# Kernel optimization log

Measured on AMD Instinct MI355X. Metric: run time of the kernel, lower is better.

## Reference

```python
import math
import jax, jax.numpy as jnp
import numpy as np

B = 64
INPUT_SIZE = 10080
PATCH = 18
S = INPUT_SIZE // PATCH  # 560 patches
E = 96                    # embed_dim
H = 12                    # num_heads
D = 96                    # head_dim == embed_dim (PAT quirk)
F = 256                   # ff_dim
L = 2                     # num_layers
EPS = 1e-5


def _sinusoidal_pe(seq_len, embed_dim):
    pos = jnp.arange(seq_len, dtype=jnp.float32)[:, None]
    div = jnp.exp(jnp.arange(0, embed_dim, 2, dtype=jnp.float32) * (-math.log(10000.0) / embed_dim))
    pe = jnp.zeros((seq_len, embed_dim), dtype=jnp.float32)
    pe = pe.at[:, 0::2].set(jnp.sin(pos * div))
    pe = pe.at[:, 1::2].set(jnp.cos(pos * div))
    return pe


def _layernorm(x, g, b):
    mu = jnp.mean(x, axis=-1, keepdims=True)
    var = jnp.var(x, axis=-1, keepdims=True)
    return (x - mu) * jax.lax.rsqrt(var + EPS) * g + b


def setup_inputs() -> dict:
    key = jax.random.key(0)
    ks = jax.random.split(key, 12)
    sd = 0.02
    inp = {
        "x": jax.random.normal(ks[0], (B, INPUT_SIZE), dtype=jnp.float32),
        "patch_W": jax.random.normal(ks[1], (PATCH, E), dtype=jnp.float32) * sd,
        "patch_b": jnp.zeros((E,), jnp.float32),
        "Wq": jax.random.normal(ks[2], (L, H, E, D), dtype=jnp.float32) * sd,
        "bq": jnp.zeros((L, H, D), jnp.float32),
        "Wk": jax.random.normal(ks[3], (L, H, E, D), dtype=jnp.float32) * sd,
        "bk": jnp.zeros((L, H, D), jnp.float32),
        "Wv": jax.random.normal(ks[4], (L, H, E, D), dtype=jnp.float32) * sd,
        "bv": jnp.zeros((L, H, D), jnp.float32),
        "Wo": jax.random.normal(ks[5], (L, H * D, E), dtype=jnp.float32) * sd,
        "bo": jnp.zeros((L, E), jnp.float32),
        "ff1_W": jax.random.normal(ks[6], (L, E, F), dtype=jnp.float32) * sd,
        "ff1_b": jnp.zeros((L, F), jnp.float32),
        "ff2_W": jax.random.normal(ks[7], (L, F, E), dtype=jnp.float32) * sd,
        "ff2_b": jnp.zeros((L, E), jnp.float32),
        "n1_g": jnp.ones((L, E), jnp.float32),
        "n1_b": jnp.zeros((L, E), jnp.float32),
        "n2_g": jnp.ones((L, E), jnp.float32),
        "n2_b": jnp.zeros((L, E), jnp.float32),
    }
    return inp


def reference(x, patch_W, patch_b, Wq, bq, Wk, bk, Wv, bv, Wo, bo,
              ff1_W, ff1_b, ff2_W, ff2_b, n1_g, n1_b, n2_g, n2_b):
    scale = 1.0 / math.sqrt(D)
    # patch embedding: [B, S, PATCH] -> [B, S, E]
    h = x.reshape(B, S, PATCH) @ patch_W + patch_b
    h = h + _sinusoidal_pe(S, E)[None]
    for l in range(L):
        # all heads at once (original loops over heads; same math)
        q = jnp.einsum('bse,hed->bhsd', h, Wq[l]) + bq[l][None, :, None, :]
        k = jnp.einsum('bse,hed->bhsd', h, Wk[l]) + bk[l][None, :, None, :]
        v = jnp.einsum('bse,hed->bhsd', h, Wv[l]) + bv[l][None, :, None, :]
        scores = jnp.einsum('bhsd,bhtd->bhst', q, k) * scale
        attn = jax.nn.softmax(scores, axis=-1)
        heads = jnp.einsum('bhst,bhtd->bhsd', attn, v)
        concat = heads.transpose(0, 2, 1, 3).reshape(B, S, H * D)
        attn_out = concat @ Wo[l] + bo[l]
        h = _layernorm(h + attn_out, n1_g[l], n1_b[l])
        ff = jax.nn.relu(h @ ff1_W[l] + ff1_b[l]) @ ff2_W[l] + ff2_b[l]
        h = _layernorm(h + ff, n2_g[l], n2_b[l])
    return h
```

## Files before the change

kernel.cpp:

```cpp
#include <hip/hip_runtime.h>
#include <hip/hip_bf16.h>
#include <math.h>

#define BATCH 64
#define CHUNK 32
#define INPUT_SIZE 10080
#define PATCH 18
#define SEQ 560
#define EMB 96
#define NHEAD 12
#define HDIM 96
#define FFDIM 256
#define NLAYER 2
#define TOK (BATCH * SEQ)
#define EPSV 1e-5f
#define SCALE 0.10206207261596577f

typedef __attribute__((ext_vector_type(8))) short bf16x8;
typedef __attribute__((ext_vector_type(4))) short bf16x4;
typedef __attribute__((ext_vector_type(4))) float f32x4;

static __device__ __forceinline__ short f2bf(float x) {
  union { __hip_bfloat16 b; short s; } u;
  u.b = __float2bfloat16(x);
  return u.s;
}

__global__ __launch_bounds__(256) void allprep_kernel(
    const float* __restrict__ Wq, const float* __restrict__ Wk,
    const float* __restrict__ Wv, const float* __restrict__ Wo,
    const float* __restrict__ ff1_W, const float* __restrict__ ff2_W,
    __hip_bfloat16* __restrict__ wqT, __hip_bfloat16* __restrict__ wkvT,
    __hip_bfloat16* __restrict__ woT, __hip_bfloat16* __restrict__ ff1WT,
    __hip_bfloat16* __restrict__ ff2WT) {
  int bx = blockIdx.x;
  if (bx < 72) {
    int hh = bx % NHEAD, mat = (bx / NHEAD) % 3, l = bx / 36;
    const float* src = (mat == 0 ? Wq : (mat == 1 ? Wk : Wv)) +
                       ((size_t)l * NHEAD + hh) * EMB * HDIM;
    __shared__ float t[HDIM * 97];
    for (int i = threadIdx.x; i < EMB * HDIM; i += 256) {
      int e = i / HDIM, d = i % HDIM;
      t[d * 97 + e] = src[i];
    }
    __syncthreads();
    __hip_bfloat16* dst;
    if (mat == 0)
      dst = wqT + ((size_t)l * NHEAD + hh) * HDIM * EMB;
    else
      dst = wkvT + ((size_t)l * 2 * NHEAD * HDIM + (mat - 1) * NHEAD * HDIM +
                    hh * HDIM) * EMB;
    for (int j = threadIdx.x; j < HDIM * EMB; j += 256) {
      int d = j / EMB, e = j % EMB;
      dst[j] = __float2bfloat16(t[d * 97 + e]);
    }
  } else if (bx < 74) {
    int l = bx - 72;
    const float* src = Wo + (size_t)l * NHEAD * HDIM * EMB;
    __hip_bfloat16* dst = woT + (size_t)l * EMB * NHEAD * HDIM;
    for (int i = threadIdx.x; i < EMB * NHEAD * HDIM; i += 256) {
      int e = i / (NHEAD * HDIM), j = i % (NHEAD * HDIM);
      dst[i] = __float2bfloat16(src[(size_t)j * EMB + e]);
    }
  } else {
    int idx = bx - 74;
    int mat = idx % 2, l = idx / 2;
    if (mat == 0) {
      const float* src = ff1_W + (size_t)l * EMB * FFDIM;
      __hip_bfloat16* dst = ff1WT + (size_t)l * FFDIM * EMB;
      for (int i = threadIdx.x; i < FFDIM * EMB; i += 256) {
        int f = i / EMB, e = i % EMB;
        dst[i] = __float2bfloat16(src[(size_t)e * FFDIM + f]);
      }
    } else {
      const float* src = ff2_W + (size_t)l * FFDIM * EMB;
      __hip_bfloat16* dst = ff2WT + (size_t)l * EMB * FFDIM;
      for (int i = threadIdx.x; i < EMB * FFDIM; i += 256) {
        int e = i / FFDIM, f = i % FFDIM;
        dst[i] = __float2bfloat16(src[(size_t)f * EMB + e]);
      }
    }
  }
}

__global__ void patch_pe_kernel(const float* __restrict__ x,
                                const float* __restrict__ W,
                                const float* __restrict__ bias,
                                float* __restrict__ h,
                                __hip_bfloat16* __restrict__ hbf) {
  int gid = blockIdx.x * blockDim.x + threadIdx.x;
  if (gid >= TOK * EMB) return;
  int tok = gid / EMB;
  int e = gid % EMB;
  int b = tok / SEQ;
  int s = tok % SEQ;
  const float* xp = x + b * INPUT_SIZE + s * PATCH;
  float acc = bias[e];
#pragma unroll
  for (int p = 0; p < PATCH; p++) acc += xp[p] * W[p * EMB + e];
  int i = e >> 1;
  float freq = __expf(-(float)(2 * i) * (9.210340371976184f / 96.0f));
  float ang = (float)s * freq;
  acc += (e & 1) ? cosf(ang) : sinf(ang);
  h[gid] = acc;
  hbf[gid] = __float2bfloat16(acc);
}

__global__ __launch_bounds__(256) void kv_mfma_kernel(
    const __hip_bfloat16* __restrict__ hbf,
    const __hip_bfloat16* __restrict__ wkvT, const float* __restrict__ bk,
    const float* __restrict__ bv, __hip_bfloat16* __restrict__ kbuf,
    __hip_bfloat16* __restrict__ vbufT, int b0) {
  const int wave = threadIdx.x >> 6;
  const int lane = threadIdx.x & 63;
  const int tq = lane & 15;
  const int quad = lane >> 4;
  const int m0 = blockIdx.x * 64 + wave * 16;
  const int n0 = blockIdx.y * 64;

  __shared__ short tile[4][16][68];

  const short* ap =
      (const short*)hbf + ((size_t)b0 * SEQ + m0 + tq) * EMB + quad * 8;
  bf16x8 a0 = *(const bf16x8*)(ap);
  bf16x8 a1 = *(const bf16x8*)(ap + 32);
  bf16x8 a2 = *(const bf16x8*)(ap + 64);

  f32x4 acc[4];
  const f32x4 zero4 = {0.f, 0.f, 0.f, 0.f};
#pragma unroll
  for (int nt = 0; nt < 4; nt++) acc[nt] = zero4;
#pragma unroll
  for (int nt = 0; nt < 4; nt++) {
    const short* bp =
        (const short*)wkvT + (size_t)(n0 + nt * 16 + tq) * EMB + quad * 8;
    bf16x8 b0f = *(const bf16x8*)(bp);
    bf16x8 b1f = *(const bf16x8*)(bp + 32);
    bf16x8 b2f = *(const bf16x8*)(bp + 64);
    acc[nt] = __builtin_amdgcn_mfma_f32_16x16x32_bf16(a0, b0f, acc[nt], 0, 0, 0);
    acc[nt] = __builtin_amdgcn_mfma_f32_16x16x32_bf16(a1, b1f, acc[nt], 0, 0, 0);
    acc[nt] = __builtin_amdgcn_mfma_f32_16x16x32_bf16(a2, b2f, acc[nt], 0, 0, 0);
  }

  const int tl0 = m0 + quad * 4;
  const int blb = tl0 / SEQ;
  const int ss0 = tl0 - blb * SEQ;

  if (n0 < NHEAD * HDIM) {
#pragma unroll
    for (int nt = 0; nt < 4; nt++) {
      int n = n0 + nt * 16 + tq;
      float bias = bk[n];
#pragma unroll
      for (int j = 0; j < 4; j++)
        tile[wave][quad * 4 + j][nt * 16 + tq] = f2bf(acc[nt][j] + bias);
    }
#pragma unroll
    for (int it = 0; it < 2; it++) {
      int idx = it * 64 + lane;
      int row = idx >> 3;
      int seg = idx & 7;
      int tl = m0 + row;
      int bb = tl / SEQ;
      int ss = tl - bb * SEQ;
      int r0s = n0 + seg * 8;
      int hh2 = r0s / HDIM;
      int d0 = r0s - hh2 * HDIM;
      bf16x8 v = *(const bf16x8*)&tile[wave][row][seg * 8];
      *(bf16x8*)((short*)kbuf +
                 ((size_t)(bb * NHEAD + hh2) * SEQ + ss) * HDIM + d0) = v;
    }
  } else {
#pragma unroll
    for (int nt = 0; nt < 4; nt++) {
      int n = n0 + nt * 16 + tq;
      int r = n - NHEAD * HDIM;
      int hh2 = r / HDIM;
      int d = r - hh2 * HDIM;
      float bias = bv[r];
      bf16x4 pack;
#pragma unroll
      for (int j = 0; j < 4; j++) pack[j] = f2bf(acc[nt][j] + bias);
      *(bf16x4*)((short*)vbufT +
                 ((size_t)(blb * NHEAD + hh2) * HDIM + d) * SEQ + ss0) = pack;
    }
  }
}

#define PSTRIDE 584
#define KSTR 104
__global__ __launch_bounds__(256, 2) void attn_mfma_kernel(
    const __hip_bfloat16* __restrict__ hbf,
    const __hip_bfloat16* __restrict__ wqT, const float* __restrict__ bq,
    const __hip_bfloat16* __restrict__ kbuf,
    const __hip_bfloat16* __restrict__ vbufT,
    __hip_bfloat16* __restrict__ heads, int b0) {
  const int flat = blockIdx.x;
  const int xcd = flat & 7;
  const int slot = flat >> 3;
  const int g = (slot / 9) * 8 + xcd;
  const int qt = slot % 9;
  const int hh = g % NHEAD;
  const int bl = g / NHEAD;
  const int wave = threadIdx.x >> 6;
  const int lane = threadIdx.x & 63;
  const int tq = lane & 15;
  const int quad = lane >> 4;

  __shared__ __align__(16) short sbuf[4 * 16 * PSTRIDE];
  short* pw = sbuf + wave * 16 * PSTRIDE;

  const size_t bh = (size_t)(bl * NHEAD + hh);
  const short* kb = (const short*)kbuf + bh * SEQ * HDIM;
  const short* vb = (const short*)vbufT + bh * HDIM * SEQ;

  const int q0 = qt * 64 + wave * 16;
  int qrow = q0 + tq;
  if (qrow > SEQ - 1) qrow = SEQ - 1;
  const short* hp =
      (const short*)hbf + ((size_t)(b0 + bl) * SEQ + qrow) * EMB + quad * 8;
  bf16x8 ha0 = *(const bf16x8*)(hp);
  bf16x8 ha1 = *(const bf16x8*)(hp + 32);
  bf16x8 ha2 = *(const bf16x8*)(hp + 64);
  const f32x4 zero4 = {0.f, 0.f, 0.f, 0.f};
  f32x4 qacc[6];
#pragma unroll
  for (int dt = 0; dt < 6; dt++) qacc[dt] = zero4;
#pragma unroll
  for (int dt = 0; dt < 6; dt++) {
    const short* wp = (const short*)wqT +
                      ((size_t)hh * HDIM + dt * 16 + tq) * EMB + quad * 8;
    bf16x8 w0 = *(const bf16x8*)(wp);
    bf16x8 w1 = *(const bf16x8*)(wp + 32);
    bf16x8 w2 = *(const bf16x8*)(wp + 64);
    qacc[dt] = __builtin_amdgcn_mfma_f32_16x16x32_bf16(ha0, w0, qacc[dt], 0, 0, 0);
    qacc[dt] = __builtin_amdgcn_mfma_f32_16x16x32_bf16(ha1, w1, qacc[dt], 0, 0, 0);
    qacc[dt] = __builtin_amdgcn_mfma_f32_16x16x32_bf16(ha2, w2, qacc[dt], 0, 0, 0);
  }
#pragma unroll
  for (int dt = 0; dt < 6; dt++) {
    int d = dt * 16 + tq;
    float bias = bq[hh * HDIM + d];
#pragma unroll
    for (int r = 0; r < 4; r++)
      pw[(quad * 4 + r) * PSTRIDE + d] = f2bf((qacc[dt][r] + bias) * SCALE);
  }
  bf16x8 aq0 = *(const bf16x8*)&pw[tq * PSTRIDE + quad * 8];
  bf16x8 aq1 = *(const bf16x8*)&pw[tq * PSTRIDE + quad * 8 + 32];
  bf16x8 aq2 = *(const bf16x8*)&pw[tq * PSTRIDE + quad * 8 + 64];
  __syncthreads();

  f32x4 acc[35];
#pragma unroll
  for (int tt = 0; tt < 35; tt++) acc[tt] = zero4;

  for (int i = threadIdx.x; i < 288 * 12; i += 256) {
    int row = i / 12, gg = i - row * 12;
    *(bf16x8*)&sbuf[row * KSTR + gg * 8] =
        *(const bf16x8*)(kb + (size_t)row * HDIM + gg * 8);
  }
  __syncthreads();
#pragma unroll
  for (int tt = 0; tt < 18; tt++) {
    const short* kp = &sbuf[(tt * 16 + tq) * KSTR + quad * 8];
    bf16x8 kb0 = *(const bf16x8*)(kp);
    bf16x8 kb1 = *(const bf16x8*)(kp + 32);
    bf16x8 kb2 = *(const bf16x8*)(kp + 64);
    acc[tt] = __builtin_amdgcn_mfma_f32_16x16x32_bf16(aq0, kb0, acc[tt], 0, 0, 0);
    acc[tt] = __builtin_amdgcn_mfma_f32_16x16x32_bf16(aq1, kb1, acc[tt], 0, 0, 0);
    acc[tt] = __builtin_amdgcn_mfma_f32_16x16x32_bf16(aq2, kb2, acc[tt], 0, 0, 0);
  }
  __syncthreads();

  for (int i = threadIdx.x; i < 272 * 12; i += 256) {
    int row = i / 12, gg = i - row * 12;
    *(bf16x8*)&sbuf[row * KSTR + gg * 8] =
        *(const bf16x8*)(kb + (size_t)(288 + row) * HDIM + gg * 8);
  }
  __syncthreads();
#pragma unroll
  for (int tt = 18; tt < 35; tt++) {
    const short* kp = &sbuf[(tt * 16 + tq - 288) * KSTR + quad * 8];
    bf16x8 kb0 = *(const bf16x8*)(kp);
    bf16x8 kb1 = *(const bf16x8*)(kp + 32);
    bf16x8 kb2 = *(const bf16x8*)(kp + 64);
    acc[tt] = __builtin_amdgcn_mfma_f32_16x16x32_bf16(aq0, kb0, acc[tt], 0, 0, 0);
    acc[tt] = __builtin_amdgcn_mfma_f32_16x16x32_bf16(aq1, kb1, acc[tt], 0, 0, 0);
    acc[tt] = __builtin_amdgcn_mfma_f32_16x16x32_bf16(aq2, kb2, acc[tt], 0, 0, 0);
  }

  float m0 = -1e30f, m1 = -1e30f, m2 = -1e30f, m3 = -1e30f;
#pragma unroll
  for (int tt = 0; tt < 35; tt++) {
    m0 = fmaxf(m0, acc[tt][0]);
    m1 = fmaxf(m1, acc[tt][1]);
    m2 = fmaxf(m2, acc[tt][2]);
    m3 = fmaxf(m3, acc[tt][3]);
  }
#pragma unroll
  for (int mask = 1; mask < 16; mask <<= 1) {
    m0 = fmaxf(m0, __shfl_xor(m0, mask, 64));
    m1 = fmaxf(m1, __shfl_xor(m1, mask, 64));
    m2 = fmaxf(m2, __shfl_xor(m2, mask, 64));
    m3 = fmaxf(m3, __shfl_xor(m3, mask, 64));
  }
  float l0 = 0.f, l1 = 0.f, l2 = 0.f, l3 = 0.f;
#pragma unroll
  for (int tt = 0; tt < 35; tt++) {
    float p0 = __expf(acc[tt][0] - m0); acc[tt][0] = p0; l0 += p0;
    float p1 = __expf(acc[tt][1] - m1); acc[tt][1] = p1; l1 += p1;
    float p2 = __expf(acc[tt][2] - m2); acc[tt][2] = p2; l2 += p2;
    float p3 = __expf(acc[tt][3] - m3); acc[tt][3] = p3; l3 += p3;
  }
#pragma unroll
  for (int mask = 1; mask < 16; mask <<= 1) {
    l0 += __shfl_xor(l0, mask, 64);
    l1 += __shfl_xor(l1, mask, 64);
    l2 += __shfl_xor(l2, mask, 64);
    l3 += __shfl_xor(l3, mask, 64);
  }
  __syncthreads();

  for (int i = lane; i < 256; i += 64)
    pw[(i >> 4) * PSTRIDE + 560 + (i & 15)] = 0;
#pragma unroll
  for (int tt = 0; tt < 35; tt++) {
    int col = tt * 16 + tq;
    pw[(quad * 4 + 0) * PSTRIDE + col] = f2bf(acc[tt][0]);
    pw[(quad * 4 + 1) * PSTRIDE + col] = f2bf(acc[tt][1]);
    pw[(quad * 4 + 2) * PSTRIDE + col] = f2bf(acc[tt][2]);
    pw[(quad * 4 + 3) * PSTRIDE + col] = f2bf(acc[tt][3]);
  }

  f32x4 oacc[6];
#pragma unroll
  for (int dt = 0; dt < 6; dt++) oacc[dt] = zero4;
#pragma unroll
  for (int kt = 0; kt < 18; kt++) {
    bf16x8 pa = *(const bf16x8*)&pw[tq * PSTRIDE + kt * 32 + quad * 8];
#pragma unroll
    for (int dt = 0; dt < 6; dt++) {
      const short* vp = vb + (size_t)(dt * 16 + tq) * SEQ + kt * 32 + quad * 8;
      bf16x8 vf = *(const bf16x8*)vp;
      oacc[dt] = __builtin_amdgcn_mfma_f32_16x16x32_bf16(pa, vf, oacc[dt], 0, 0, 0);
    }
  }

  float r0 = 1.f / l0, r1 = 1.f / l1, r2 = 1.f / l2, r3 = 1.f / l3;
  int qg = q0 + quad * 4;
  __hip_bfloat16* hpout =
      heads + ((size_t)(b0 + bl) * SEQ) * (NHEAD * HDIM) + (size_t)hh * HDIM;
#pragma unroll
  for (int dt = 0; dt < 6; dt++) {
    int d = dt * 16 + tq;
    if (qg + 0 < SEQ) hpout[(size_t)(qg + 0) * (NHEAD * HDIM) + d] = __float2bfloat16(oacc[dt][0] * r0);
    if (qg + 1 < SEQ) hpout[(size_t)(qg + 1) * (NHEAD * HDIM) + d] = __float2bfloat16(oacc[dt][1] * r1);
    if (qg + 2 < SEQ) hpout[(size_t)(qg + 2) * (NHEAD * HDIM) + d] = __float2bfloat16(oacc[dt][2] * r2);
    if (qg + 3 < SEQ) hpout[(size_t)(qg + 3) * (NHEAD * HDIM) + d] = __float2bfloat16(oacc[dt][3] * r3);
  }
}

__global__ __launch_bounds__(256) void wo_ln_mfma_kernel(
    const __hip_bfloat16* __restrict__ heads,
    const __hip_bfloat16* __restrict__ woT, const float* __restrict__ bo,
    const float* __restrict__ gamma, const float* __restrict__ beta,
    const float* __restrict__ hres, float* __restrict__ hA,
    __hip_bfloat16* __restrict__ hbf) {
  const int wave = threadIdx.x >> 6;
  const int lane = threadIdx.x & 63;
  const int tq = lane & 15;
  const int quad = lane >> 4;
  const int m0 = blockIdx.x * 64 + wave * 16;

  const short* ap = (const short*)heads + (size_t)(m0 + tq) * (NHEAD * HDIM);
  const short* bp = (const short*)woT;

  f32x4 acc[6];
  const f32x4 zero4 = {0.f, 0.f, 0.f, 0.f};
#pragma unroll
  for (int dt = 0; dt < 6; dt++) acc[dt] = zero4;

  for (int kt = 0; kt < 36; kt++) {
    bf16x8 af = *(const bf16x8*)(ap + kt * 32 + quad * 8);
#pragma unroll
    for (int dt = 0; dt < 6; dt++) {
      bf16x8 bfr = *(const bf16x8*)(bp + (size_t)(dt * 16 + tq) * (NHEAD * HDIM) +
                                    kt * 32 + quad * 8);
      acc[dt] = __builtin_amdgcn_mfma_f32_16x16x32_bf16(af, bfr, acc[dt], 0, 0, 0);
    }
  }

  const int tok0 = m0 + quad * 4;
  float s1[4] = {0.f, 0.f, 0.f, 0.f};
  float s2[4] = {0.f, 0.f, 0.f, 0.f};
#pragma unroll
  for (int dt = 0; dt < 6; dt++) {
    int n = dt * 16 + tq;
    float bias = bo[n];
#pragma unroll
    for (int r = 0; r < 4; r++) {
      float val = acc[dt][r] + bias + hres[(size_t)(tok0 + r) * EMB + n];
      acc[dt][r] = val;
      s1[r] += val;
      s2[r] += val * val;
    }
  }
#pragma unroll
  for (int mask = 1; mask < 16; mask <<= 1) {
#pragma unroll
    for (int r = 0; r < 4; r++) {
      s1[r] += __shfl_xor(s1[r], mask, 64);
      s2[r] += __shfl_xor(s2[r], mask, 64);
    }
  }
  float mean[4], rstd[4];
#pragma unroll
  for (int r = 0; r < 4; r++) {
    mean[r] = s1[r] * (1.0f / EMB);
    float var = s2[r] * (1.0f / EMB) - mean[r] * mean[r];
    rstd[r] = rsqrtf(var + EPSV);
  }
#pragma unroll
  for (int dt = 0; dt < 6; dt++) {
    int n = dt * 16 + tq;
    float g = gamma[n], bt = beta[n];
#pragma unroll
    for (int r = 0; r < 4; r++) {
      float o = (acc[dt][r] - mean[r]) * rstd[r] * g + bt;
      hA[(size_t)(tok0 + r) * EMB + n] = o;
      hbf[(size_t)(tok0 + r) * EMB + n] = __float2bfloat16(o);
    }
  }
}

__global__ __launch_bounds__(256) void ff1_mfma_kernel(
    const __hip_bfloat16* __restrict__ hbf,
    const __hip_bfloat16* __restrict__ ff1WT, const float* __restrict__ b1,
    __hip_bfloat16* __restrict__ ffbf) {
  const int wave = threadIdx.x >> 6;
  const int lane = threadIdx.x & 63;
  const int tq = lane & 15;
  const int quad = lane >> 4;
  const int m0 = blockIdx.x * 64 + wave * 16;

  const short* ap = (const short*)hbf + (size_t)(m0 + tq) * EMB + quad * 8;
  bf16x8 a0 = *(const bf16x8*)(ap);
  bf16x8 a1 = *(const bf16x8*)(ap + 32);
  bf16x8 a2 = *(const bf16x8*)(ap + 64);

  f32x4 acc[16];
  const f32x4 zero4 = {0.f, 0.f, 0.f, 0.f};
#pragma unroll
  for (int nt = 0; nt < 16; nt++) acc[nt] = zero4;
#pragma unroll
  for (int nt = 0; nt < 16; nt++) {
    const short* bp =
        (const short*)ff1WT + (size_t)(nt * 16 + tq) * EMB + quad * 8;
    bf16x8 b0f = *(const bf16x8*)(bp);
    bf16x8 b1f = *(const bf16x8*)(bp + 32);
    bf16x8 b2f = *(const bf16x8*)(bp + 64);
    acc[nt] = __builtin_amdgcn_mfma_f32_16x16x32_bf16(a0, b0f, acc[nt], 0, 0, 0);
    acc[nt] = __builtin_amdgcn_mfma_f32_16x16x32_bf16(a1, b1f, acc[nt], 0, 0, 0);
    acc[nt] = __builtin_amdgcn_mfma_f32_16x16x32_bf16(a2, b2f, acc[nt], 0, 0, 0);
  }

  const int tok0 = m0 + quad * 4;
#pragma unroll
  for (int nt = 0; nt < 16; nt++) {
    int n = nt * 16 + tq;
    float bias = b1[n];
#pragma unroll
    for (int r = 0; r < 4; r++) {
      ffbf[(size_t)(tok0 + r) * FFDIM + n] =
          __float2bfloat16(fmaxf(acc[nt][r] + bias, 0.f));
    }
  }
}

__global__ __launch_bounds__(256) void ff2_ln_mfma_kernel(
    const __hip_bfloat16* __restrict__ ffbf,
    const __hip_bfloat16* __restrict__ ff2WT, const float* __restrict__ b2,
    const float* __restrict__ gamma, const float* __restrict__ beta,
    const float* __restrict__ hres, float* __restrict__ hout,
    __hip_bfloat16* __restrict__ hbf_out) {
  const int wave = threadIdx.x >> 6;
  const int lane = threadIdx.x & 63;
  const int tq = lane & 15;
  const int quad = lane >> 4;
  const int m0 = blockIdx.x * 64 + wave * 16;

  const short* ap = (const short*)ffbf + (size_t)(m0 + tq) * FFDIM;
  const short* bp = (const short*)ff2WT;

  f32x4 acc[6];
  const f32x4 zero4 = {0.f, 0.f, 0.f, 0.f};
#pragma unroll
  for (int dt = 0; dt < 6; dt++) acc[dt] = zero4;

#pragma unroll
  for (int kt = 0; kt < 8; kt++) {
    bf16x8 af = *(const bf16x8*)(ap + kt * 32 + quad * 8);
#pragma unroll
    for (int dt = 0; dt < 6; dt++) {
      bf16x8 bfr = *(const bf16x8*)(bp + (size_t)(dt * 16 + tq) * FFDIM +
                                    kt * 32 + quad * 8);
      acc[dt] = __builtin_amdgcn_mfma_f32_16x16x32_bf16(af, bfr, acc[dt], 0, 0, 0);
    }
  }

  const int tok0 = m0 + quad * 4;
  float s1[4] = {0.f, 0.f, 0.f, 0.f};
  float s2[4] = {0.f, 0.f, 0.f, 0.f};
#pragma unroll
  for (int dt = 0; dt < 6; dt++) {
    int n = dt * 16 + tq;
    float bias = b2[n];
#pragma unroll
    for (int r = 0; r < 4; r++) {
      float val = acc[dt][r] + bias + hres[(size_t)(tok0 + r) * EMB + n];
      acc[dt][r] = val;
      s1[r] += val;
      s2[r] += val * val;
    }
  }
#pragma unroll
  for (int mask = 1; mask < 16; mask <<= 1) {
#pragma unroll
    for (int r = 0; r < 4; r++) {
      s1[r] += __shfl_xor(s1[r], mask, 64);
      s2[r] += __shfl_xor(s2[r], mask, 64);
    }
  }
  float mean[4], rstd[4];
#pragma unroll
  for (int r = 0; r < 4; r++) {
    mean[r] = s1[r] * (1.0f / EMB);
    float var = s2[r] * (1.0f / EMB) - mean[r] * mean[r];
    rstd[r] = rsqrtf(var + EPSV);
  }
#pragma unroll
  for (int dt = 0; dt < 6; dt++) {
    int n = dt * 16 + tq;
    float g = gamma[n], bt = beta[n];
#pragma unroll
    for (int r = 0; r < 4; r++) {
      float o = (acc[dt][r] - mean[r]) * rstd[r] * g + bt;
      hout[(size_t)(tok0 + r) * EMB + n] = o;
      hbf_out[(size_t)(tok0 + r) * EMB + n] = __float2bfloat16(o);
    }
  }
}

extern "C" void kernel_launch(void* const* d_in, const int* in_sizes, int n_in,
                              void* d_out, int out_size, void* d_ws,
                              size_t ws_size, hipStream_t stream) {
  const float* x = (const float*)d_in[0];
  const float* patch_W = (const float*)d_in[1];
  const float* patch_b = (const float*)d_in[2];
  const float* Wq = (const float*)d_in[3];
  const float* bq = (const float*)d_in[4];
  const float* Wk = (const float*)d_in[5];
  const float* bk = (const float*)d_in[6];
  const float* Wv = (const float*)d_in[7];
  const float* bv = (const float*)d_in[8];
  const float* Wo = (const float*)d_in[9];
  const float* bo = (const float*)d_in[10];
  const float* ff1_W = (const float*)d_in[11];
  const float* ff1_b = (const float*)d_in[12];
  const float* ff2_W = (const float*)d_in[13];
  const float* ff2_b = (const float*)d_in[14];
  const float* n1_g = (const float*)d_in[15];
  const float* n1_b = (const float*)d_in[16];
  const float* n2_g = (const float*)d_in[17];
  const float* n2_b = (const float*)d_in[18];

  const size_t h_bytes = (size_t)TOK * EMB * sizeof(float);
  const size_t hbf_bytes = (size_t)TOK * EMB * 2;
  const size_t kv_bytes = (size_t)CHUNK * NHEAD * SEQ * HDIM * 2;
  const size_t heads_bytes = (size_t)TOK * NHEAD * HDIM * 2;
  const size_t wqT_bytes = (size_t)NLAYER * NHEAD * HDIM * EMB * 2;
  const size_t wkvT_bytes = 2 * wqT_bytes;
  const size_t woT_bytes = (size_t)NLAYER * EMB * NHEAD * HDIM * 2;
  const size_t ffw_bytes = (size_t)NLAYER * FFDIM * EMB * 2;
  char* ws = (char*)d_ws;
  size_t off = 0;
  float* h = (float*)(ws + off); off += h_bytes;
  float* hA = (float*)(ws + off); off += h_bytes;
  __hip_bfloat16* hbf = (__hip_bfloat16*)(ws + off); off += hbf_bytes;
  __hip_bfloat16* kbuf = (__hip_bfloat16*)(ws + off); off += kv_bytes;
  __hip_bfloat16* vbufT = (__hip_bfloat16*)(ws + off); off += kv_bytes;
  __hip_bfloat16* heads = (__hip_bfloat16*)(ws + off); off += heads_bytes;
  __hip_bfloat16* wqT = (__hip_bfloat16*)(ws + off); off += wqT_bytes;
  __hip_bfloat16* wkvT = (__hip_bfloat16*)(ws + off); off += wkvT_bytes;
  __hip_bfloat16* woT = (__hip_bfloat16*)(ws + off); off += woT_bytes;
  __hip_bfloat16* ff1WT = (__hip_bfloat16*)(ws + off); off += ffw_bytes;
  __hip_bfloat16* ff2WT = (__hip_bfloat16*)(ws + off); off += ffw_bytes;
  __hip_bfloat16* ffbf = (__hip_bfloat16*)kbuf;

  allprep_kernel<<<78, 256, 0, stream>>>(Wq, Wk, Wv, Wo, ff1_W, ff2_W, wqT,
                                         wkvT, woT, ff1WT, ff2WT);
  patch_pe_kernel<<<(TOK * EMB + 255) / 256, 256, 0, stream>>>(x, patch_W,
                                                               patch_b, h, hbf);

  for (int l = 0; l < NLAYER; l++) {
    const __hip_bfloat16* wqT_l = wqT + (size_t)l * NHEAD * HDIM * EMB;
    const __hip_bfloat16* wkvT_l = wkvT + (size_t)l * 2 * NHEAD * HDIM * EMB;
    const __hip_bfloat16* woT_l = woT + (size_t)l * EMB * NHEAD * HDIM;
    const __hip_bfloat16* ff1WT_l = ff1WT + (size_t)l * FFDIM * EMB;
    const __hip_bfloat16* ff2WT_l = ff2WT + (size_t)l * EMB * FFDIM;
    const float* bq_l = bq + (size_t)l * NHEAD * HDIM;
    const float* bk_l = bk + (size_t)l * NHEAD * HDIM;
    const float* bv_l = bv + (size_t)l * NHEAD * HDIM;
    const float* bo_l = bo + (size_t)l * EMB;

    for (int c = 0; c < BATCH / CHUNK; c++) {
      int b0 = c * CHUNK;
      kv_mfma_kernel<<<dim3(CHUNK * SEQ / 64, 2 * NHEAD * HDIM / 64), 256, 0,
                       stream>>>(hbf, wkvT_l, bk_l, bv_l, kbuf, vbufT, b0);
      attn_mfma_kernel<<<9 * NHEAD * CHUNK, 256, 0, stream>>>(
          hbf, wqT_l, bq_l, kbuf, vbufT, heads, b0);
    }
    wo_ln_mfma_kernel<<<TOK / 64, 256, 0, stream>>>(
        heads, woT_l, bo_l, n1_g + l * EMB, n1_b + l * EMB, h, hA, hbf);
    ff1_mfma_kernel<<<TOK / 64, 256, 0, stream>>>(hbf, ff1WT_l,
                                                  ff1_b + l * FFDIM, ffbf);
    float* dst = (l == NLAYER - 1) ? (float*)d_out : h;
    ff2_ln_mfma_kernel<<<TOK / 64, 256, 0, stream>>>(
        ffbf, ff2WT_l, ff2_b + l * EMB, n2_g + l * EMB, n2_b + l * EMB, hA,
        dst, hbf);
  }
}
```

Measured before the change: 1.382 ms.

## Replace two-pass attention with online-softmax flash kernel over 64-key chunks

Rewrites the attention kernel as a flash-style loop over 64-key chunks with an online softmax, so the 35-tile score accumulator array and the full 560-wide probability buffer in LDS are no longer needed. Each wave now handles two 16-row query tiles, so every K and V fragment read from global feeds twice as many MFMAs. LDS per block shrinks enough to target three blocks per CU, and the grid drops to 5 query tiles per head. In exchange, it adds per-chunk max and rescale work, reads K straight from global instead of staging it in LDS, and masks the padded last chunk.

```diff
diff --git a/kernel.cpp b/kernel.cpp
--- a/kernel.cpp
+++ b/kernel.cpp
@@ -187,9 +187,9 @@
   }
 }
 
-#define PSTRIDE 584
-#define KSTR 104
-__global__ __launch_bounds__(256, 2) void attn_mfma_kernel(
+#define QW 104
+#define PW 72
+__global__ __launch_bounds__(256, 3) void attn_flash_kernel(
     const __hip_bfloat16* __restrict__ hbf,
     const __hip_bfloat16* __restrict__ wqT, const float* __restrict__ bq,
     const __hip_bfloat16* __restrict__ kbuf,
@@ -198,8 +198,8 @@
   const int flat = blockIdx.x;
   const int xcd = flat & 7;
   const int slot = flat >> 3;
-  const int g = (slot / 9) * 8 + xcd;
-  const int qt = slot % 9;
+  const int g = (slot / 5) * 8 + xcd;
+  const int qt = slot % 5;
   const int hh = g % NHEAD;
   const int bl = g / NHEAD;
   const int wave = threadIdx.x >> 6;
@@ -207,25 +207,31 @@
   const int tq = lane & 15;
   const int quad = lane >> 4;
 
-  __shared__ __align__(16) short sbuf[4 * 16 * PSTRIDE];
-  short* pw = sbuf + wave * 16 * PSTRIDE;
+  __shared__ __align__(16) short sbuf[4][3328];
+  short* pw = sbuf[wave];
 
   const size_t bh = (size_t)(bl * NHEAD + hh);
   const short* kb = (const short*)kbuf + bh * SEQ * HDIM;
   const short* vb = (const short*)vbufT + bh * HDIM * SEQ;
 
-  const int q0 = qt * 64 + wave * 16;
-  int qrow = q0 + tq;
-  if (qrow > SEQ - 1) qrow = SEQ - 1;
-  const short* hp =
-      (const short*)hbf + ((size_t)(b0 + bl) * SEQ + qrow) * EMB + quad * 8;
-  bf16x8 ha0 = *(const bf16x8*)(hp);
-  bf16x8 ha1 = *(const bf16x8*)(hp + 32);
-  bf16x8 ha2 = *(const bf16x8*)(hp + 64);
+  const int q0 = qt * 128 + wave * 32;
+
+  int qrA = q0 + tq;      if (qrA > SEQ - 1) qrA = SEQ - 1;
+  int qrB = q0 + 16 + tq; if (qrB > SEQ - 1) qrB = SEQ - 1;
+  const short* hpA =
+      (const short*)hbf + ((size_t)(b0 + bl) * SEQ + qrA) * EMB + quad * 8;
+  const short* hpB =
+      (const short*)hbf + ((size_t)(b0 + bl) * SEQ + qrB) * EMB + quad * 8;
+  bf16x8 haA0 = *(const bf16x8*)(hpA);
+  bf16x8 haA1 = *(const bf16x8*)(hpA + 32);
+  bf16x8 haA2 = *(const bf16x8*)(hpA + 64);
+  bf16x8 haB0 = *(const bf16x8*)(hpB);
+  bf16x8 haB1 = *(const bf16x8*)(hpB + 32);
+  bf16x8 haB2 = *(const bf16x8*)(hpB + 64);
   const f32x4 zero4 = {0.f, 0.f, 0.f, 0.f};
-  f32x4 qacc[6];
-#pragma unroll
-  for (int dt = 0; dt < 6; dt++) qacc[dt] = zero4;
+  f32x4 qaccA[6], qaccB[6];
+#pragma unroll
+  for (int dt = 0; dt < 6; dt++) { qaccA[dt] = zero4; qaccB[dt] = zero4; }
 #pragma unroll
   for (int dt = 0; dt < 6; dt++) {
     const short* wp = (const short*)wqT +
@@ -233,130 +239,147 @@
     bf16x8 w0 = *(const bf16x8*)(wp);
     bf16x8 w1 = *(const bf16x8*)(wp + 32);
     bf16x8 w2 = *(const bf16x8*)(wp + 64);
-    qacc[dt] = __builtin_amdgcn_mfma_f32_16x16x32_bf16(ha0, w0, qacc[dt], 0, 0, 0);
-    qacc[dt] = __builtin_amdgcn_mfma_f32_16x16x32_bf16(ha1, w1, qacc[dt], 0, 0, 0);
-    qacc[dt] = __builtin_amdgcn_mfma_f32_16x16x32_bf16(ha2, w2, qacc[dt], 0, 0, 0);
+    qaccA[dt] = __builtin_amdgcn_mfma_f32_16x16x32_bf16(haA0, w0, qaccA[dt], 0, 0, 0);
+    qaccA[dt] = __builtin_amdgcn_mfma_f32_16x16x32_bf16(haA1, w1, qaccA[dt], 0, 0, 0);
+    qaccA[dt] = __builtin_amdgcn_mfma_f32_16x16x32_bf16(haA2, w2, qaccA[dt], 0, 0, 0);
+    qaccB[dt] = __builtin_amdgcn_mfma_f32_16x16x32_bf16(haB0, w0, qaccB[dt], 0, 0, 0);
+    qaccB[dt] = __builtin_amdgcn_mfma_f32_16x16x32_bf16(haB1, w1, qaccB[dt], 0, 0, 0);
+    qaccB[dt] = __builtin_amdgcn_mfma_f32_16x16x32_bf16(haB2, w2, qaccB[dt], 0, 0, 0);
   }
 #pragma unroll
   for (int dt = 0; dt < 6; dt++) {
     int d = dt * 16 + tq;
     float bias = bq[hh * HDIM + d];
 #pragma unroll
+    for (int r = 0; r < 4; r++) {
+      pw[(quad * 4 + r) * QW + d] = f2bf((qaccA[dt][r] + bias) * SCALE);
+      pw[(16 + quad * 4 + r) * QW + d] = f2bf((qaccB[dt][r] + bias) * SCALE);
+    }
+  }
+  bf16x8 aqA0 = *(const bf16x8*)&pw[tq * QW + quad * 8];
+  bf16x8 aqA1 = *(const bf16x8*)&pw[tq * QW + 32 + quad * 8];
+  bf16x8 aqA2 = *(const bf16x8*)&pw[tq * QW + 64 + quad * 8];
+  bf16x8 aqB0 = *(const bf16x8*)&pw[(16 + tq) * QW + quad * 8];
+  bf16x8 aqB1 = *(const bf16x8*)&pw[(16 + tq) * QW + 32 + quad * 8];
+  bf16x8 aqB2 = *(const bf16x8*)&pw[(16 + tq) * QW + 64 + quad * 8];
+
+  f32x4 oA[6], oB[6];
+#pragma unroll
+  for (int dt = 0; dt < 6; dt++) { oA[dt] = zero4; oB[dt] = zero4; }
+  float mA[4], mB[4], lA[4], lB[4];
+#pragma unroll
+  for (int r = 0; r < 4; r++) {
+    mA[r] = -1e30f; mB[r] = -1e30f; lA[r] = 0.f; lB[r] = 0.f;
+  }
+
+  for (int c = 0; c < 9; c++) {
+    const int col0 = c * 64;
+    f32x4 sA[4], sB[4];
+#pragma unroll
+    for (int t = 0; t < 4; t++) { sA[t] = zero4; sB[t] = zero4; }
+#pragma unroll
+    for (int t = 0; t < 4; t++) {
+      const short* kp = kb + (size_t)(col0 + t * 16 + tq) * HDIM + quad * 8;
+      bf16x8 k0 = *(const bf16x8*)(kp);
+      bf16x8 k1 = *(const bf16x8*)(kp + 32);
+      bf16x8 k2 = *(const bf16x8*)(kp + 64);
+      sA[t] = __builtin_amdgcn_mfma_f32_16x16x32_bf16(aqA0, k0, sA[t], 0, 0, 0);
+      sA[t] = __builtin_amdgcn_mfma_f32_16x16x32_bf16(aqA1, k1, sA[t], 0, 0, 0);
+      sA[t] = __builtin_amdgcn_mfma_f32_16x16x32_bf16(aqA2, k2, sA[t], 0, 0, 0);
+      sB[t] = __builtin_amdgcn_mfma_f32_16x16x32_bf16(aqB0, k0, sB[t], 0, 0, 0);
+      sB[t] = __builtin_amdgcn_mfma_f32_16x16x32_bf16(aqB1, k1, sB[t], 0, 0, 0);
+      sB[t] = __builtin_amdgcn_mfma_f32_16x16x32_bf16(aqB2, k2, sB[t], 0, 0, 0);
+    }
+    if (c == 8) {
+#pragma unroll
+      for (int r = 0; r < 4; r++) { sA[3][r] = -1e30f; sB[3][r] = -1e30f; }
+    }
+    float cA[4], cB[4];
+#pragma unroll
+    for (int r = 0; r < 4; r++) {
+      cA[r] = fmaxf(fmaxf(sA[0][r], sA[1][r]), fmaxf(sA[2][r], sA[3][r]));
+      cB[r] = fmaxf(fmaxf(sB[0][r], sB[1][r]), fmaxf(sB[2][r], sB[3][r]));
+    }
+#pragma unroll
+    for (int mask = 1; mask < 16; mask <<= 1) {
+#pragma unroll
+      for (int r = 0; r < 4; r++) {
+        cA[r] = fmaxf(cA[r], __shfl_xor(cA[r], mask, 64));
+        cB[r] = fmaxf(cB[r], __shfl_xor(cB[r], mask, 64));
+      }
+    }
+    bool need = false;
+#pragma unroll
     for (int r = 0; r < 4; r++)
-      pw[(quad * 4 + r) * PSTRIDE + d] = f2bf((qacc[dt][r] + bias) * SCALE);
-  }
-  bf16x8 aq0 = *(const bf16x8*)&pw[tq * PSTRIDE + quad * 8];
-  bf16x8 aq1 = *(const bf16x8*)&pw[tq * PSTRIDE + quad * 8 + 32];
-  bf16x8 aq2 = *(const bf16x8*)&pw[tq * PSTRIDE + quad * 8 + 64];
-  __syncthreads();
-
-  f32x4 acc[35];
-#pragma unroll
-  for (int tt = 0; tt < 35; tt++) acc[tt] = zero4;
-
-  for (int i = threadIdx.x; i < 288 * 12; i += 256) {
-    int row = i / 12, gg = i - row * 12;
-    *(bf16x8*)&sbuf[row * KSTR + gg * 8] =
-        *(const bf16x8*)(kb + (size_t)row * HDIM + gg * 8);
-  }
-  __syncthreads();
-#pragma unroll
-  for (int tt = 0; tt < 18; tt++) {
-    const short* kp = &sbuf[(tt * 16 + tq) * KSTR + quad * 8];
-    bf16x8 kb0 = *(const bf16x8*)(kp);
-    bf16x8 kb1 = *(const bf16x8*)(kp + 32);
-    bf16x8 kb2 = *(const bf16x8*)(kp + 64);
-    acc[tt] = __builtin_amdgcn_mfma_f32_16x16x32_bf16(aq0, kb0, acc[tt], 0, 0, 0);
-    acc[tt] = __builtin_amdgcn_mfma_f32_16x16x32_bf16(aq1, kb1, acc[tt], 0, 0, 0);
-    acc[tt] = __builtin_amdgcn_mfma_f32_16x16x32_bf16(aq2, kb2, acc[tt], 0, 0, 0);
-  }
-  __syncthreads();
-
-  for (int i = threadIdx.x; i < 272 * 12; i += 256) {
-    int row = i / 12, gg = i - row * 12;
-    *(bf16x8*)&sbuf[row * KSTR + gg * 8] =
-        *(const bf16x8*)(kb + (size_t)(288 + row) * HDIM + gg * 8);
-  }
-  __syncthreads();
-#pragma unroll
-  for (int tt = 18; tt < 35; tt++) {
-    const short* kp = &sbuf[(tt * 16 + tq - 288) * KSTR + quad * 8];
-    bf16x8 kb0 = *(const bf16x8*)(kp);
-    bf16x8 kb1 = *(const bf16x8*)(kp + 32);
-    bf16x8 kb2 = *(const bf16x8*)(kp + 64);
-    acc[tt] = __builtin_amdgcn_mfma_f32_16x16x32_bf16(aq0, kb0, acc[tt], 0, 0, 0);
-    acc[tt] = __builtin_amdgcn_mfma_f32_16x16x32_bf16(aq1, kb1, acc[tt], 0, 0, 0);
-    acc[tt] = __builtin_amdgcn_mfma_f32_16x16x32_bf16(aq2, kb2, acc[tt], 0, 0, 0);
-  }
-
-  float m0 = -1e30f, m1 = -1e30f, m2 = -1e30f, m3 = -1e30f;
-#pragma unroll
-  for (int tt = 0; tt < 35; tt++) {
-    m0 = fmaxf(m0, acc[tt][0]);
-    m1 = fmaxf(m1, acc[tt][1]);
-    m2 = fmaxf(m2, acc[tt][2]);
-    m3 = fmaxf(m3, acc[tt][3]);
-  }
+      need = need | (cA[r] > mA[r]) | (cB[r] > mB[r]);
+    if (__any(need)) {
+#pragma unroll
+      for (int r = 0; r < 4; r++) {
+        float mnA = fmaxf(mA[r], cA[r]);
+        float fA = __expf(mA[r] - mnA);
+        mA[r] = mnA; lA[r] *= fA;
+        float mnB = fmaxf(mB[r], cB[r]);
+        float fB = __expf(mB[r] - mnB);
+        mB[r] = mnB; lB[r] *= fB;
+#pragma unroll
+        for (int dt = 0; dt < 6; dt++) { oA[dt][r] *= fA; oB[dt][r] *= fB; }
+      }
+    }
+#pragma unroll
+    for (int t = 0; t < 4; t++) {
+#pragma unroll
+      for (int r = 0; r < 4; r++) {
+        float pA = __expf(sA[t][r] - mA[r]);
+        lA[r] += pA;
+        pw[(quad * 4 + r) * PW + t * 16 + tq] = f2bf(pA);
+        float pB = __expf(sB[t][r] - mB[r]);
+        lB[r] += pB;
+        pw[(16 + quad * 4 + r) * PW + t * 16 + tq] = f2bf(pB);
+      }
+    }
+    bf16x8 paA0 = *(const bf16x8*)&pw[tq * PW + quad * 8];
+    bf16x8 paA1 = *(const bf16x8*)&pw[tq * PW + 32 + quad * 8];
+    bf16x8 paB0 = *(const bf16x8*)&pw[(16 + tq) * PW + quad * 8];
+    bf16x8 paB1 = *(const bf16x8*)&pw[(16 + tq) * PW + 32 + quad * 8];
+#pragma unroll
+    for (int dt = 0; dt < 6; dt++) {
+      const short* vp = vb + (size_t)(dt * 16 + tq) * SEQ + col0 + quad * 8;
+      bf16x8 v0 = *(const bf16x8*)(vp);
+      bf16x8 v1 = *(const bf16x8*)(vp + 32);
+      oA[dt] = __builtin_amdgcn_mfma_f32_16x16x32_bf16(paA0, v0, oA[dt], 0, 0, 0);
+      oA[dt] = __builtin_amdgcn_mfma_f32_16x16x32_bf16(paA1, v1, oA[dt], 0, 0, 0);
+      oB[dt] = __builtin_amdgcn_mfma_f32_16x16x32_bf16(paB0, v0, oB[dt], 0, 0, 0);
+      oB[dt] = __builtin_amdgcn_mfma_f32_16x16x32_bf16(paB1, v1, oB[dt], 0, 0, 0);
+    }
+  }
+
 #pragma unroll
   for (int mask = 1; mask < 16; mask <<= 1) {
-    m0 = fmaxf(m0, __shfl_xor(m0, mask, 64));
-    m1 = fmaxf(m1, __shfl_xor(m1, mask, 64));
-    m2 = fmaxf(m2, __shfl_xor(m2, mask, 64));
-    m3 = fmaxf(m3, __shfl_xor(m3, mask, 64));
-  }
-  float l0 = 0.f, l1 = 0.f, l2 = 0.f, l3 = 0.f;
-#pragma unroll
-  for (int tt = 0; tt < 35; tt++) {
-    float p0 = __expf(acc[tt][0] - m0); acc[tt][0] = p0; l0 += p0;
-    float p1 = __expf(acc[tt][1] - m1); acc[tt][1] = p1; l1 += p1;
-    float p2 = __expf(acc[tt][2] - m2); acc[tt][2] = p2; l2 += p2;
-    float p3 = __expf(acc[tt][3] - m3); acc[tt][3] = p3; l3 += p3;
-  }
-#pragma unroll
-  for (int mask = 1; mask < 16; mask <<= 1) {
-    l0 += __shfl_xor(l0, mask, 64);
-    l1 += __shfl_xor(l1, mask, 64);
-    l2 += __shfl_xor(l2, mask, 64);
-    l3 += __shfl_xor(l3, mask, 64);
-  }
-  __syncthreads();
-
-  for (int i = lane; i < 256; i += 64)
-    pw[(i >> 4) * PSTRIDE + 560 + (i & 15)] = 0;
-#pragma unroll
-  for (int tt = 0; tt < 35; tt++) {
-    int col = tt * 16 + tq;
-    pw[(quad * 4 + 0) * PSTRIDE + col] = f2bf(acc[tt][0]);
-    pw[(quad * 4 + 1) * PSTRIDE + col] = f2bf(acc[tt][1]);
-    pw[(quad * 4 + 2) * PSTRIDE + col] = f2bf(acc[tt][2]);
-    pw[(quad * 4 + 3) * PSTRIDE + col] = f2bf(acc[tt][3]);
-  }
-
-  f32x4 oacc[6];
-#pragma unroll
-  for (int dt = 0; dt < 6; dt++) oacc[dt] = zero4;
-#pragma unroll
-  for (int kt = 0; kt < 18; kt++) {
-    bf16x8 pa = *(const bf16x8*)&pw[tq * PSTRIDE + kt * 32 + quad * 8];
-#pragma unroll
-    for (int dt = 0; dt < 6; dt++) {
-      const short* vp = vb + (size_t)(dt * 16 + tq) * SEQ + kt * 32 + quad * 8;
-      bf16x8 vf = *(const bf16x8*)vp;
-      oacc[dt] = __builtin_amdgcn_mfma_f32_16x16x32_bf16(pa, vf, oacc[dt], 0, 0, 0);
-    }
-  }
-
-  float r0 = 1.f / l0, r1 = 1.f / l1, r2 = 1.f / l2, r3 = 1.f / l3;
-  int qg = q0 + quad * 4;
+#pragma unroll
+    for (int r = 0; r < 4; r++) {
+      lA[r] += __shfl_xor(lA[r], mask, 64);
+      lB[r] += __shfl_xor(lB[r], mask, 64);
+    }
+  }
+  float rA[4], rB[4];
+#pragma unroll
+  for (int r = 0; r < 4; r++) { rA[r] = 1.f / lA[r]; rB[r] = 1.f / lB[r]; }
   __hip_bfloat16* hpout =
       heads + ((size_t)(b0 + bl) * SEQ) * (NHEAD * HDIM) + (size_t)hh * HDIM;
+  const int qgA = q0 + quad * 4;
+  const int qgB = q0 + 16 + quad * 4;
 #pragma unroll
   for (int dt = 0; dt < 6; dt++) {
     int d = dt * 16 + tq;
-    if (qg + 0 < SEQ) hpout[(size_t)(qg + 0) * (NHEAD * HDIM) + d] = __float2bfloat16(oacc[dt][0] * r0);
-    if (qg + 1 < SEQ) hpout[(size_t)(qg + 1) * (NHEAD * HDIM) + d] = __float2bfloat16(oacc[dt][1] * r1);
-    if (qg + 2 < SEQ) hpout[(size_t)(qg + 2) * (NHEAD * HDIM) + d] = __float2bfloat16(oacc[dt][2] * r2);
-    if (qg + 3 < SEQ) hpout[(size_t)(qg + 3) * (NHEAD * HDIM) + d] = __float2bfloat16(oacc[dt][3] * r3);
+#pragma unroll
+    for (int r = 0; r < 4; r++) {
+      if (qgA + r < SEQ)
+        hpout[(size_t)(qgA + r) * (NHEAD * HDIM) + d] =
+            __float2bfloat16(oA[dt][r] * rA[r]);
+      if (qgB + r < SEQ)
+        hpout[(size_t)(qgB + r) * (NHEAD * HDIM) + d] =
+            __float2bfloat16(oB[dt][r] * rB[r]);
+    }
   }
 }
 
@@ -617,7 +640,7 @@
       int b0 = c * CHUNK;
       kv_mfma_kernel<<<dim3(CHUNK * SEQ / 64, 2 * NHEAD * HDIM / 64), 256, 0,
                        stream>>>(hbf, wkvT_l, bk_l, bv_l, kbuf, vbufT, b0);
-      attn_mfma_kernel<<<9 * NHEAD * CHUNK, 256, 0, stream>>>(
+      attn_flash_kernel<<<5 * NHEAD * CHUNK, 256, 0, stream>>>(
           hbf, wqT_l, bq_l, kbuf, vbufT, heads, b0);
     }
     wo_ln_mfma_kernel<<<TOK / 64, 256, 0, stream>>>(
```

After: 1.251 ms. 9.4% less time.
